# Performance work log

Hardware: AMD Instinct MI355X
Metric: run time of the kernel (lower is better)

Reference implementation:

```python
import jax, jax.numpy as jnp
import numpy as np

LAYER_START = 4
WS = 2  # context_window_size
EPS = 1e-8


def _alpha_for_k(tf, idx):
    # tf: [L, D] per-token layer features; idx: static window row indices (last entry is k)
    Wm = tf[idx]                       # [w, D]
    w = Wm.shape[0]
    _, R = jnp.linalg.qr(Wm.T)         # reduced QR of [D, w] -> R: [w, w]
    r = R[:, -1]
    sub = R[:-1, :-1]
    coln = jnp.linalg.norm(sub, axis=0)
    align = jnp.mean(sub / coln, axis=1) @ R[:-1, -1] / jnp.linalg.norm(r[:-1])
    align = 1.0 / (align * w * 2)
    nov = jnp.abs(r[-1]) / jnp.linalg.norm(r)
    return align, nov


def _unify_token(tf):
    # tf: [L, D] -> pooled [D]
    L = tf.shape[0]
    aligns, novs = [], []
    for k in range(L):  # loop over small fixed layer count (structurally distinct windows)
        # NOTE: original torch code token_feature[k-ws:k] yields an EMPTY slice for k < ws
        left = list(range(k - WS, k)) if k >= WS else []
        right = list(range(k + 1, min(k + WS + 1, L)))
        idx = np.array(left + right + [k], dtype=np.int32)
        a, n = _alpha_for_k(tf, idx)
        aligns.append(a)
        novs.append(n)
    aa = jnp.stack(aligns)
    nv = jnp.stack(novs)
    aa = aa / aa.sum()
    nv = nv / nv.sum()
    alpha = aa + nv
    alpha = alpha / alpha.sum()
    return tf.T @ alpha


def _token_var(tf):
    # tf: [L, D] -> variance (unbiased) of subdiagonal of cosine-sim map
    w = jnp.linalg.norm(tf, axis=1, keepdims=True)
    sim = (tf @ tf.T) / jnp.clip(w * w.T, EPS)
    return jnp.var(jnp.diagonal(sim, -1), ddof=1)


def reference(all_hidden_states, attention_mask):
    # all_hidden_states: [B, num_layers, S, D]; attention_mask: [B, S] (all sentences equal length)
    T = int(np.asarray(attention_mask).sum(axis=1)[0]) - 1  # unmask_num = sum(mask) - 1
    sf = all_hidden_states[:, LAYER_START:, :T, :]          # [B, L, T, D]
    per_tok = jax.vmap(jax.vmap(_unify_token, in_axes=1))(sf)  # [B, T, D]

    def per_sentence(s, ose):
        v = jax.vmap(_token_var, in_axes=1)(s)  # [T]
        v = v / v.sum()
        return ose.T @ v                        # [D]

    return jax.vmap(per_sentence)(sf, per_tok)  # [B, D]


def setup_inputs():
    key = jax.random.key(0)
    all_hidden_states = jax.random.normal(key, (8, 12, 512, 768), dtype=jnp.float32)
    attention_mask = jnp.ones((8, 512), dtype=jnp.int32)
    return {"all_hidden_states": all_hidden_states, "attention_mask": attention_mask}
```

## Files before the change

kernel.cpp:

```cpp
#include <hip/hip_runtime.h>
#include <math.h>

#define NLAYER_TOT 12
#define LAYER0 4
#define SMAX 512
#define DIM 768
#define NSEG 128

__host__ __device__ constexpr int gp(int i, int j) {
    return (i <= j) ? (i * 8 - i * (i - 1) / 2 + (j - i))
                    : (j * 8 - j * (j - 1) / 2 + (i - j));
}

__device__ inline float frcp(float x) { return __builtin_amdgcn_rcpf(x); }
__device__ inline float frsq(float x) { return __builtin_amdgcn_rsqf(x); }

__device__ inline float wave_reduce_add(float v) {
    v += __int_as_float(__builtin_amdgcn_update_dpp(0, __float_as_int(v), 0x121, 0xF, 0xF, true));
    v += __int_as_float(__builtin_amdgcn_update_dpp(0, __float_as_int(v), 0x122, 0xF, 0xF, true));
    v += __int_as_float(__builtin_amdgcn_update_dpp(0, __float_as_int(v), 0x124, 0xF, 0xF, true));
    v += __int_as_float(__builtin_amdgcn_update_dpp(0, __float_as_int(v), 0x128, 0xF, 0xF, true));
    v += __shfl_xor(v, 16, 64);
    v += __shfl_xor(v, 32, 64);
    return v;
}

__global__ void k_init(const int* __restrict__ mask, int* __restrict__ wsT) {
    __shared__ int red[512];
    int tid = threadIdx.x;
    red[tid] = mask[tid];
    __syncthreads();
    for (int s = 256; s >= 1; s >>= 1) {
        if (tid < s) red[tid] += red[tid + s];
        __syncthreads();
    }
    if (tid == 0) wsT[0] = red[0] - 1;
}

template <int W>
__device__ inline void alpha_nov(const float (&A)[36], const int (&idx)[5],
                                 float& align_o, float& nov_o) {
    float Gs[W][W];
#pragma unroll
    for (int i = 0; i < W; ++i)
#pragma unroll
        for (int j = i; j < W; ++j) {
            float v = A[gp(idx[i], idx[j])];
            Gs[i][j] = v;
            Gs[j][i] = v;
        }
    float R[W][W];
#pragma unroll
    for (int j = 0; j < W; ++j) {
#pragma unroll
        for (int i = 0; i <= j; ++i) {
            float s = Gs[i][j];
#pragma unroll
            for (int q = 0; q < i; ++q) s -= R[q][i] * R[q][j];
            if (i == j) R[i][j] = s * frsq(s);
            else        R[i][j] = s * frcp(R[i][i]);
        }
    }
    float ic[W - 1];
#pragma unroll
    for (int j = 0; j < W - 1; ++j) ic[j] = frsq(Gs[j][j]);
    float m[W - 1];
#pragma unroll
    for (int i = 0; i < W - 1; ++i) {
        float s = 0.0f;
#pragma unroll
        for (int j = i; j < W - 1; ++j) s += R[i][j] * ic[j];
        m[i] = s * (1.0f / (float)(W - 1));
    }
    float num = 0.0f, n1 = 0.0f;
#pragma unroll
    for (int i = 0; i < W - 1; ++i) {
        num += m[i] * R[i][W - 1];
        n1 += R[i][W - 1] * R[i][W - 1];
    }
    float align_raw = num * frsq(n1);
    align_o = frcp(align_raw * (float)W * 2.0f);
    nov_o = fabsf(R[W - 1][W - 1]) * frsq(Gs[W - 1][W - 1]);
}

__global__ __launch_bounds__(256, 2) void k_main(const float* __restrict__ in,
                                                 const int* __restrict__ wsT,
                                                 float* __restrict__ P,
                                                 float* __restrict__ Vp) {
    int T = wsT[0];
    int seg = blockIdx.x;
    int b = blockIdx.y;
    int wave = threadIdx.x >> 6;
    int lane = threadIdx.x & 63;

    __shared__ float part[DIM];
    __shared__ float vpart;
    for (int i = threadIdx.x; i < DIM; i += 256) part[i] = 0.0f;
    if (threadIdx.x == 0) vpart = 0.0f;
    __syncthreads();

    int t = seg * 4 + wave;
    float4 acc12[3];
#pragma unroll
    for (int it = 0; it < 3; ++it) acc12[it] = make_float4(0.f, 0.f, 0.f, 0.f);
    float vloc = 0.0f;

    if (t < T) {
        const float* base = in + ((size_t)(b * NLAYER_TOT + LAYER0) * SMAX + t) * DIM;

        float g[36];
#pragma unroll
        for (int p = 0; p < 36; ++p) g[p] = 0.0f;
        float4 cur[8], nxt[8];
#pragma unroll
        for (int k = 0; k < 8; ++k)
            cur[k] = *(const float4*)(base + (size_t)k * SMAX * DIM + lane * 4);
#pragma unroll
        for (int it = 0; it < 3; ++it) {
            if (it < 2) {
                int d = (it + 1) * 256 + lane * 4;
#pragma unroll
                for (int k = 0; k < 8; ++k)
                    nxt[k] = *(const float4*)(base + (size_t)k * SMAX * DIM + d);
            }
            int p = 0;
#pragma unroll
            for (int i = 0; i < 8; ++i)
#pragma unroll
                for (int j = i; j < 8; ++j) {
                    g[p] += cur[i].x * cur[j].x + cur[i].y * cur[j].y +
                            cur[i].z * cur[j].z + cur[i].w * cur[j].w;
                    ++p;
                }
            if (it < 2) {
#pragma unroll
                for (int k = 0; k < 8; ++k) cur[k] = nxt[k];
            }
        }
#pragma unroll
        for (int p = 0; p < 36; ++p) g[p] = wave_reduce_add(g[p]);

#pragma unroll
        for (int k = 0; k < 8; ++k)
            cur[k] = *(const float4*)(base + (size_t)k * SMAX * DIM + lane * 4);

        static constexpr int IDX0[5] = {1, 2, 0, 0, 0};
        static constexpr int IDX1[5] = {2, 3, 1, 0, 0};
        static constexpr int IDX2[5] = {0, 1, 3, 4, 2};
        static constexpr int IDX3[5] = {1, 2, 4, 5, 3};
        static constexpr int IDX4[5] = {2, 3, 5, 6, 4};
        static constexpr int IDX5[5] = {3, 4, 6, 7, 5};
        static constexpr int IDX6[5] = {4, 5, 7, 6, 0};
        static constexpr int IDX7[5] = {5, 6, 7, 0, 0};
        float a[8], n[8];
        alpha_nov<3>(g, IDX0, a[0], n[0]);
        alpha_nov<3>(g, IDX1, a[1], n[1]);
        alpha_nov<5>(g, IDX2, a[2], n[2]);
        alpha_nov<5>(g, IDX3, a[3], n[3]);
        alpha_nov<5>(g, IDX4, a[4], n[4]);
        alpha_nov<5>(g, IDX5, a[5], n[5]);
        alpha_nov<4>(g, IDX6, a[6], n[6]);
        alpha_nov<3>(g, IDX7, a[7], n[7]);
        float sa = 0.0f, sn = 0.0f;
#pragma unroll
        for (int k = 0; k < 8; ++k) { sa += a[k]; sn += n[k]; }
        float isa = frcp(sa), isn = frcp(sn);
        float al[8], ss = 0.0f;
#pragma unroll
        for (int k = 0; k < 8; ++k) { al[k] = a[k] * isa + n[k] * isn; ss += al[k]; }
        float iss = frcp(ss);
        float c[7], mu = 0.0f;
#pragma unroll
        for (int i = 0; i < 7; ++i) {
            float denom = g[gp(i, i)] * g[gp(i + 1, i + 1)];
            c[i] = g[gp(i, i + 1)] * frsq(denom > 1e-16f ? denom : 1e-16f);
            mu += c[i];
        }
        mu *= (1.0f / 7.0f);
        float var = 0.0f;
#pragma unroll
        for (int i = 0; i < 7; ++i) var += (c[i] - mu) * (c[i] - mu);
        float vraw = var * (1.0f / 6.0f);
        vloc = vraw;
        float p8[8];
#pragma unroll
        for (int k = 0; k < 8; ++k) p8[k] = al[k] * iss * vraw;

#pragma unroll
        for (int it = 0; it < 3; ++it) {
            if (it < 2) {
                int d = (it + 1) * 256 + lane * 4;
#pragma unroll
                for (int k = 0; k < 8; ++k)
                    nxt[k] = *(const float4*)(base + (size_t)k * SMAX * DIM + d);
            }
#pragma unroll
            for (int k = 0; k < 8; ++k) {
                acc12[it].x += p8[k] * cur[k].x;
                acc12[it].y += p8[k] * cur[k].y;
                acc12[it].z += p8[k] * cur[k].z;
                acc12[it].w += p8[k] * cur[k].w;
            }
            if (it < 2) {
#pragma unroll
                for (int k = 0; k < 8; ++k) cur[k] = nxt[k];
            }
        }

#pragma unroll
        for (int it = 0; it < 3; ++it) {
            int d = it * 256 + lane * 4;
            atomicAdd(&part[d + 0], acc12[it].x);
            atomicAdd(&part[d + 1], acc12[it].y);
            atomicAdd(&part[d + 2], acc12[it].z);
            atomicAdd(&part[d + 3], acc12[it].w);
        }
        if (lane == 0) atomicAdd(&vpart, vloc);
    }
    __syncthreads();

    float* pd = P + ((size_t)b * NSEG + seg) * DIM;
    for (int i = threadIdx.x; i < DIM; i += 256) pd[i] = part[i];
    if (threadIdx.x == 0) Vp[b * NSEG + seg] = vpart;
}

__global__ void k_reduce(const float* __restrict__ P, const float* __restrict__ Vp,
                         float* __restrict__ out) {
    int b = blockIdx.x;
    int d = threadIdx.x;
    __shared__ float vred[NSEG];
    __shared__ float vinv;
    if (d < NSEG) vred[d] = Vp[b * NSEG + d];
    __syncthreads();
    if (d == 0) {
        float s = 0.0f;
        for (int i = 0; i < NSEG; ++i) s += vred[i];
        vinv = 1.0f / s;
    }
    __syncthreads();
    float s = 0.0f;
    const float* pb = P + (size_t)b * NSEG * DIM;
    for (int seg = 0; seg < NSEG; ++seg) s += pb[(size_t)seg * DIM + d];
    out[b * DIM + d] = s * vinv;
}

extern "C" void kernel_launch(void* const* d_in, const int* in_sizes, int n_in,
                              void* d_out, int out_size, void* d_ws, size_t ws_size,
                              hipStream_t stream) {
    const float* hs = (const float*)d_in[0];
    const int* mask = (const int*)d_in[1];
    float* out = (float*)d_out;
    char* ws = (char*)d_ws;
    int* wsT = (int*)ws;
    float* P = (float*)(ws + 256);
    float* Vp = (float*)(ws + 256 + (size_t)8 * NSEG * DIM * 4);

    k_init<<<1, 512, 0, stream>>>(mask, wsT);
    k_main<<<dim3(NSEG, 8), 256, 0, stream>>>(hs, wsT, P, Vp);
    k_reduce<<<8, DIM, 0, stream>>>(P, Vp, out);
}
```

Before: 224.1 us.

## Fuse mask reduction, main pass and final reduce into one flag-synchronized kernel

Merges the three launches into a single kernel. Every block recomputes the token count from the mask, and one extra block per batch spin-waits on per-segment release/acquire flags before summing the partials. The Cholesky loop is reordered by row so each diagonal reciprocal is computed once, and the launch bounds are raised to 4 blocks per CU. Flags are never reset between calls, so later invocations may read partials before they are rewritten. The design also depends on all blocks being co-resident to avoid a spin stall.

Measured after the change: 473.0 us. +111.0%, slower.

```diff
diff --git a/kernel.cpp b/kernel.cpp
--- a/kernel.cpp
+++ b/kernel.cpp
@@ -6,6 +6,7 @@
 #define SMAX 512
 #define DIM 768
 #define NSEG 128
+#define MAGIC 0x13579BDF
 
 __host__ __device__ constexpr int gp(int i, int j) {
     return (i <= j) ? (i * 8 - i * (i - 1) / 2 + (j - i))
@@ -25,18 +26,6 @@
     return v;
 }
 
-__global__ void k_init(const int* __restrict__ mask, int* __restrict__ wsT) {
-    __shared__ int red[512];
-    int tid = threadIdx.x;
-    red[tid] = mask[tid];
-    __syncthreads();
-    for (int s = 256; s >= 1; s >>= 1) {
-        if (tid < s) red[tid] += red[tid + s];
-        __syncthreads();
-    }
-    if (tid == 0) wsT[0] = red[0] - 1;
-}
-
 template <int W>
 __device__ inline void alpha_nov(const float (&A)[36], const int (&idx)[5],
                                  float& align_o, float& nov_o) {
@@ -51,14 +40,19 @@
         }
     float R[W][W];
 #pragma unroll
-    for (int j = 0; j < W; ++j) {
-#pragma unroll
-        for (int i = 0; i <= j; ++i) {
-            float s = Gs[i][j];
-#pragma unroll
-            for (int q = 0; q < i; ++q) s -= R[q][i] * R[q][j];
-            if (i == j) R[i][j] = s * frsq(s);
-            else        R[i][j] = s * frcp(R[i][i]);
+    for (int i = 0; i < W; ++i) {
+        float s = Gs[i][i];
+#pragma unroll
+        for (int q = 0; q < i; ++q) s -= R[q][i] * R[q][i];
+        float rs = frsq(s);
+        R[i][i] = s * rs;
+        float ir = frcp(R[i][i]);
+#pragma unroll
+        for (int j = i + 1; j < W; ++j) {
+            float s2 = Gs[i][j];
+#pragma unroll
+            for (int q = 0; q < i; ++q) s2 -= R[q][i] * R[q][j];
+            R[i][j] = s2 * ir;
         }
     }
     float ic[W - 1];
@@ -83,165 +77,188 @@
     nov_o = fabsf(R[W - 1][W - 1]) * frsq(Gs[W - 1][W - 1]);
 }
 
-__global__ __launch_bounds__(256, 2) void k_main(const float* __restrict__ in,
-                                                 const int* __restrict__ wsT,
-                                                 float* __restrict__ P,
-                                                 float* __restrict__ Vp) {
-    int T = wsT[0];
-    int seg = blockIdx.x;
+__global__ __launch_bounds__(256, 4) void k_all(const float* __restrict__ in,
+                                                const int* __restrict__ mask,
+                                                float* __restrict__ P,
+                                                float* __restrict__ Vp,
+                                                int* __restrict__ flag,
+                                                float* __restrict__ out) {
+    int x = blockIdx.x;
     int b = blockIdx.y;
-    int wave = threadIdx.x >> 6;
-    int lane = threadIdx.x & 63;
-
+    int tid = threadIdx.x;
+    int wave = tid >> 6;
+    int lane = tid & 63;
+
+    __shared__ int tred[256];
     __shared__ float part[DIM];
     __shared__ float vpart;
-    for (int i = threadIdx.x; i < DIM; i += 256) part[i] = 0.0f;
-    if (threadIdx.x == 0) vpart = 0.0f;
-    __syncthreads();
-
-    int t = seg * 4 + wave;
-    float4 acc12[3];
-#pragma unroll
-    for (int it = 0; it < 3; ++it) acc12[it] = make_float4(0.f, 0.f, 0.f, 0.f);
-    float vloc = 0.0f;
-
-    if (t < T) {
-        const float* base = in + ((size_t)(b * NLAYER_TOT + LAYER0) * SMAX + t) * DIM;
-
-        float g[36];
-#pragma unroll
-        for (int p = 0; p < 36; ++p) g[p] = 0.0f;
-        float4 cur[8], nxt[8];
-#pragma unroll
-        for (int k = 0; k < 8; ++k)
-            cur[k] = *(const float4*)(base + (size_t)k * SMAX * DIM + lane * 4);
-#pragma unroll
-        for (int it = 0; it < 3; ++it) {
-            if (it < 2) {
-                int d = (it + 1) * 256 + lane * 4;
-#pragma unroll
-                for (int k = 0; k < 8; ++k)
-                    nxt[k] = *(const float4*)(base + (size_t)k * SMAX * DIM + d);
-            }
-            int p = 0;
-#pragma unroll
-            for (int i = 0; i < 8; ++i)
-#pragma unroll
-                for (int j = i; j < 8; ++j) {
-                    g[p] += cur[i].x * cur[j].x + cur[i].y * cur[j].y +
-                            cur[i].z * cur[j].z + cur[i].w * cur[j].w;
-                    ++p;
-                }
-            if (it < 2) {
-#pragma unroll
-                for (int k = 0; k < 8; ++k) cur[k] = nxt[k];
-            }
-        }
-#pragma unroll
-        for (int p = 0; p < 36; ++p) g[p] = wave_reduce_add(g[p]);
-
-#pragma unroll
-        for (int k = 0; k < 8; ++k)
-            cur[k] = *(const float4*)(base + (size_t)k * SMAX * DIM + lane * 4);
-
-        static constexpr int IDX0[5] = {1, 2, 0, 0, 0};
-        static constexpr int IDX1[5] = {2, 3, 1, 0, 0};
-        static constexpr int IDX2[5] = {0, 1, 3, 4, 2};
-        static constexpr int IDX3[5] = {1, 2, 4, 5, 3};
-        static constexpr int IDX4[5] = {2, 3, 5, 6, 4};
-        static constexpr int IDX5[5] = {3, 4, 6, 7, 5};
-        static constexpr int IDX6[5] = {4, 5, 7, 6, 0};
-        static constexpr int IDX7[5] = {5, 6, 7, 0, 0};
-        float a[8], n[8];
-        alpha_nov<3>(g, IDX0, a[0], n[0]);
-        alpha_nov<3>(g, IDX1, a[1], n[1]);
-        alpha_nov<5>(g, IDX2, a[2], n[2]);
-        alpha_nov<5>(g, IDX3, a[3], n[3]);
-        alpha_nov<5>(g, IDX4, a[4], n[4]);
-        alpha_nov<5>(g, IDX5, a[5], n[5]);
-        alpha_nov<4>(g, IDX6, a[6], n[6]);
-        alpha_nov<3>(g, IDX7, a[7], n[7]);
-        float sa = 0.0f, sn = 0.0f;
-#pragma unroll
-        for (int k = 0; k < 8; ++k) { sa += a[k]; sn += n[k]; }
-        float isa = frcp(sa), isn = frcp(sn);
-        float al[8], ss = 0.0f;
-#pragma unroll
-        for (int k = 0; k < 8; ++k) { al[k] = a[k] * isa + n[k] * isn; ss += al[k]; }
-        float iss = frcp(ss);
-        float c[7], mu = 0.0f;
-#pragma unroll
-        for (int i = 0; i < 7; ++i) {
-            float denom = g[gp(i, i)] * g[gp(i + 1, i + 1)];
-            c[i] = g[gp(i, i + 1)] * frsq(denom > 1e-16f ? denom : 1e-16f);
-            mu += c[i];
-        }
-        mu *= (1.0f / 7.0f);
-        float var = 0.0f;
-#pragma unroll
-        for (int i = 0; i < 7; ++i) var += (c[i] - mu) * (c[i] - mu);
-        float vraw = var * (1.0f / 6.0f);
-        vloc = vraw;
-        float p8[8];
-#pragma unroll
-        for (int k = 0; k < 8; ++k) p8[k] = al[k] * iss * vraw;
-
-#pragma unroll
-        for (int it = 0; it < 3; ++it) {
-            if (it < 2) {
-                int d = (it + 1) * 256 + lane * 4;
-#pragma unroll
-                for (int k = 0; k < 8; ++k)
-                    nxt[k] = *(const float4*)(base + (size_t)k * SMAX * DIM + d);
-            }
-#pragma unroll
-            for (int k = 0; k < 8; ++k) {
-                acc12[it].x += p8[k] * cur[k].x;
-                acc12[it].y += p8[k] * cur[k].y;
-                acc12[it].z += p8[k] * cur[k].z;
-                acc12[it].w += p8[k] * cur[k].w;
-            }
-            if (it < 2) {
-#pragma unroll
-                for (int k = 0; k < 8; ++k) cur[k] = nxt[k];
-            }
-        }
-
-#pragma unroll
-        for (int it = 0; it < 3; ++it) {
-            int d = it * 256 + lane * 4;
-            atomicAdd(&part[d + 0], acc12[it].x);
-            atomicAdd(&part[d + 1], acc12[it].y);
-            atomicAdd(&part[d + 2], acc12[it].z);
-            atomicAdd(&part[d + 3], acc12[it].w);
-        }
-        if (lane == 0) atomicAdd(&vpart, vloc);
-    }
-    __syncthreads();
-
-    float* pd = P + ((size_t)b * NSEG + seg) * DIM;
-    for (int i = threadIdx.x; i < DIM; i += 256) pd[i] = part[i];
-    if (threadIdx.x == 0) Vp[b * NSEG + seg] = vpart;
-}
-
-__global__ void k_reduce(const float* __restrict__ P, const float* __restrict__ Vp,
-                         float* __restrict__ out) {
-    int b = blockIdx.x;
-    int d = threadIdx.x;
     __shared__ float vred[NSEG];
     __shared__ float vinv;
-    if (d < NSEG) vred[d] = Vp[b * NSEG + d];
+
+    tred[tid] = mask[tid] + mask[tid + 256];
     __syncthreads();
-    if (d == 0) {
-        float s = 0.0f;
-        for (int i = 0; i < NSEG; ++i) s += vred[i];
-        vinv = 1.0f / s;
-    }
-    __syncthreads();
-    float s = 0.0f;
-    const float* pb = P + (size_t)b * NSEG * DIM;
-    for (int seg = 0; seg < NSEG; ++seg) s += pb[(size_t)seg * DIM + d];
-    out[b * DIM + d] = s * vinv;
+    for (int s = 128; s >= 1; s >>= 1) {
+        if (tid < s) tred[tid] += tred[tid + s];
+        __syncthreads();
+    }
+    int T = tred[0] - 1;
+
+    if (x < NSEG) {
+        for (int i = tid; i < DIM; i += 256) part[i] = 0.0f;
+        if (tid == 0) vpart = 0.0f;
+        __syncthreads();
+
+        int t = x * 4 + wave;
+        if (t < T) {
+            const float* base = in + ((size_t)(b * NLAYER_TOT + LAYER0) * SMAX + t) * DIM;
+
+            float g[36];
+#pragma unroll
+            for (int p = 0; p < 36; ++p) g[p] = 0.0f;
+            float4 cur[8], nxt[8];
+#pragma unroll
+            for (int k = 0; k < 8; ++k)
+                cur[k] = *(const float4*)(base + (size_t)k * SMAX * DIM + lane * 4);
+#pragma unroll
+            for (int it = 0; it < 3; ++it) {
+                if (it < 2) {
+                    int d = (it + 1) * 256 + lane * 4;
+#pragma unroll
+                    for (int k = 0; k < 8; ++k)
+                        nxt[k] = *(const float4*)(base + (size_t)k * SMAX * DIM + d);
+                }
+                int p = 0;
+#pragma unroll
+                for (int i = 0; i < 8; ++i)
+#pragma unroll
+                    for (int j = i; j < 8; ++j) {
+                        g[p] += cur[i].x * cur[j].x + cur[i].y * cur[j].y +
+                                cur[i].z * cur[j].z + cur[i].w * cur[j].w;
+                        ++p;
+                    }
+                if (it < 2) {
+#pragma unroll
+                    for (int k = 0; k < 8; ++k) cur[k] = nxt[k];
+                }
+            }
+#pragma unroll
+            for (int p = 0; p < 36; ++p) g[p] = wave_reduce_add(g[p]);
+
+#pragma unroll
+            for (int k = 0; k < 8; ++k)
+                cur[k] = *(const float4*)(base + (size_t)k * SMAX * DIM + lane * 4);
+
+            static constexpr int IDX0[5] = {1, 2, 0, 0, 0};
+            static constexpr int IDX1[5] = {2, 3, 1, 0, 0};
+            static constexpr int IDX2[5] = {0, 1, 3, 4, 2};
+            static constexpr int IDX3[5] = {1, 2, 4, 5, 3};
+            static constexpr int IDX4[5] = {2, 3, 5, 6, 4};
+            static constexpr int IDX5[5] = {3, 4, 6, 7, 5};
+            static constexpr int IDX6[5] = {4, 5, 7, 6, 0};
+            static constexpr int IDX7[5] = {5, 6, 7, 0, 0};
+            float a[8], n[8];
+            alpha_nov<3>(g, IDX0, a[0], n[0]);
+            alpha_nov<3>(g, IDX1, a[1], n[1]);
+            alpha_nov<5>(g, IDX2, a[2], n[2]);
+            alpha_nov<5>(g, IDX3, a[3], n[3]);
+            alpha_nov<5>(g, IDX4, a[4], n[4]);
+            alpha_nov<5>(g, IDX5, a[5], n[5]);
+            alpha_nov<4>(g, IDX6, a[6], n[6]);
+            alpha_nov<3>(g, IDX7, a[7], n[7]);
+            float sa = 0.0f, sn = 0.0f;
+#pragma unroll
+            for (int k = 0; k < 8; ++k) { sa += a[k]; sn += n[k]; }
+            float isa = frcp(sa), isn = frcp(sn);
+            float al[8], ss = 0.0f;
+#pragma unroll
+            for (int k = 0; k < 8; ++k) { al[k] = a[k] * isa + n[k] * isn; ss += al[k]; }
+            float iss = frcp(ss);
+            float c[7], mu = 0.0f;
+#pragma unroll
+            for (int i = 0; i < 7; ++i) {
+                float denom = g[gp(i, i)] * g[gp(i + 1, i + 1)];
+                c[i] = g[gp(i, i + 1)] * frsq(denom > 1e-16f ? denom : 1e-16f);
+                mu += c[i];
+            }
+            mu *= (1.0f / 7.0f);
+            float var = 0.0f;
+#pragma unroll
+            for (int i = 0; i < 7; ++i) var += (c[i] - mu) * (c[i] - mu);
+            float vraw = var * (1.0f / 6.0f);
+            float p8[8];
+#pragma unroll
+            for (int k = 0; k < 8; ++k) p8[k] = al[k] * iss * vraw;
+
+            float4 acc12[3];
+#pragma unroll
+            for (int it = 0; it < 3; ++it) acc12[it] = make_float4(0.f, 0.f, 0.f, 0.f);
+#pragma unroll
+            for (int it = 0; it < 3; ++it) {
+                if (it < 2) {
+                    int d = (it + 1) * 256 + lane * 4;
+#pragma unroll
+                    for (int k = 0; k < 8; ++k)
+                        nxt[k] = *(const float4*)(base + (size_t)k * SMAX * DIM + d);
+                }
+#pragma unroll
+                for (int k = 0; k < 8; ++k) {
+                    acc12[it].x += p8[k] * cur[k].x;
+                    acc12[it].y += p8[k] * cur[k].y;
+                    acc12[it].z += p8[k] * cur[k].z;
+                    acc12[it].w += p8[k] * cur[k].w;
+                }
+                if (it < 2) {
+#pragma unroll
+                    for (int k = 0; k < 8; ++k) cur[k] = nxt[k];
+                }
+            }
+
+#pragma unroll
+            for (int it = 0; it < 3; ++it) {
+                int d = it * 256 + lane * 4;
+                atomicAdd(&part[d + 0], acc12[it].x);
+                atomicAdd(&part[d + 1], acc12[it].y);
+                atomicAdd(&part[d + 2], acc12[it].z);
+                atomicAdd(&part[d + 3], acc12[it].w);
+            }
+            if (lane == 0) atomicAdd(&vpart, vraw);
+        }
+        __syncthreads();
+
+        float* pd = P + ((size_t)b * NSEG + x) * DIM;
+        for (int i = tid; i < DIM; i += 256) pd[i] = part[i];
+        if (tid == 0) Vp[b * NSEG + x] = vpart;
+        __threadfence();
+        __syncthreads();
+        if (tid == 0)
+            __hip_atomic_store(&flag[b * NSEG + x], MAGIC, __ATOMIC_RELEASE,
+                               __HIP_MEMORY_SCOPE_AGENT);
+    } else {
+        if (tid < NSEG) {
+            int guard = 0;
+            while (__hip_atomic_load(&flag[b * NSEG + tid], __ATOMIC_ACQUIRE,
+                                     __HIP_MEMORY_SCOPE_AGENT) != MAGIC) {
+                if (++guard > (1 << 27)) break;
+            }
+        }
+        __syncthreads();
+        __threadfence();
+        if (tid < NSEG) vred[tid] = Vp[b * NSEG + tid];
+        __syncthreads();
+        if (tid == 0) {
+            float s = 0.0f;
+            for (int i = 0; i < NSEG; ++i) s += vred[i];
+            vinv = 1.0f / s;
+        }
+        __syncthreads();
+        const float* pb = P + (size_t)b * NSEG * DIM;
+        for (int d = tid; d < DIM; d += 256) {
+            float s = 0.0f;
+#pragma unroll 8
+            for (int seg = 0; seg < NSEG; ++seg) s += pb[(size_t)seg * DIM + d];
+            out[b * DIM + d] = s * vinv;
+        }
+    }
 }
 
 extern "C" void kernel_launch(void* const* d_in, const int* in_sizes, int n_in,
@@ -251,11 +268,9 @@
     const int* mask = (const int*)d_in[1];
     float* out = (float*)d_out;
     char* ws = (char*)d_ws;
-    int* wsT = (int*)ws;
-    float* P = (float*)(ws + 256);
-    float* Vp = (float*)(ws + 256 + (size_t)8 * NSEG * DIM * 4);
-
-    k_init<<<1, 512, 0, stream>>>(mask, wsT);
-    k_main<<<dim3(NSEG, 8), 256, 0, stream>>>(hs, wsT, P, Vp);
-    k_reduce<<<8, DIM, 0, stream>>>(P, Vp, out);
-}
+    int* flag = (int*)ws;
+    float* Vp = (float*)(ws + (size_t)8 * NSEG * 4);
+    float* P = (float*)(ws + (size_t)8 * NSEG * 8);
+
+    k_all<<<dim3(NSEG + 1, 8), 256, 0, stream>>>(hs, mask, P, Vp, flag, out);
+}
```
